# Performance work log

Hardware: AMD Instinct MI355X
Metric: run time of the kernel (lower is better)

The kernel has to match this reference:

```python
import jax, jax.numpy as jnp
import numpy as np

B, L = 64, 2048
V, E, G = 30, 128, 8          # n_tokens, embedding_size, n_globals
C, F, O = 64, 128, 30         # res_channels, f_channels, n_outputs
K, ND = 2, 9                  # kernel_size, n_dilations
GE = G * E                    # flattened global embedding dim


def causal_conv(x, w, b, dilation):
    # x: [B,Cin,L], w: [Cout,Cin,K] -> [B,Cout,L], causal via left padding
    pad = (w.shape[-1] - 1) * dilation
    out = jax.lax.conv_general_dilated(
        x, w, window_strides=(1,), padding=[(pad, 0)],
        rhs_dilation=(dilation,), dimension_numbers=("NCH", "OIH", "NCH"))
    return out + b[None, :, None]


def setup_inputs() -> dict:
    key = jax.random.key(0)
    ks = jax.random.split(key, 20)
    s = 0.05
    inp = {
        "input_tensor": jax.random.randint(ks[0], (B, L), 0, V),
        "global_input": jax.random.randint(ks[1], (B, G), 0, V),
        "emb_table": jax.random.normal(ks[2], (V, E), jnp.float32) * s,
        "w_causal": jax.random.normal(ks[3], (C, E, K), jnp.float32) * s,
        "b_causal": jnp.zeros((C,), jnp.float32),
        "w_f": jax.random.normal(ks[4], (ND, C, C, K), jnp.float32) * s,
        "b_f": jnp.zeros((ND, C), jnp.float32),
        "w_g": jax.random.normal(ks[5], (ND, C, C, K), jnp.float32) * s,
        "b_g": jnp.zeros((ND, C), jnp.float32),
        "wl_f": jax.random.normal(ks[6], (ND, C, GE), jnp.float32) * s,
        "bl_f": jnp.zeros((ND, C), jnp.float32),
        "wl_g": jax.random.normal(ks[7], (ND, C, GE), jnp.float32) * s,
        "bl_g": jnp.zeros((ND, C), jnp.float32),
        "w_res": jax.random.normal(ks[8], (ND, C, C), jnp.float32) * s,
        "b_res": jnp.zeros((ND, C), jnp.float32),
        "w_fin1": jax.random.normal(ks[9], (F, C), jnp.float32) * s,
        "b_fin1": jnp.zeros((F,), jnp.float32),
        "w_fin2": jax.random.normal(ks[10], (O, F), jnp.float32) * s,
        "b_fin2": jnp.zeros((O,), jnp.float32),
    }
    return inp


def reference(input_tensor, global_input, emb_table, w_causal, b_causal,
              w_f, b_f, w_g, b_g, wl_f, bl_f, wl_g, bl_g,
              w_res, b_res, w_fin1, b_fin1, w_fin2, b_fin2):
    # padding_idx=0: row 0 is zero and receives no gradient
    table = emb_table.at[0].set(0.0)
    emb = table[input_tensor]                     # [B,L,E]
    emb_g = table[global_input].reshape(B, GE)    # [B,G*E]
    x = jnp.transpose(emb, (0, 2, 1))             # [B,E,L]
    res = causal_conv(x, w_causal, b_causal, 1)   # [B,C,L]
    skips = jnp.zeros_like(res)
    for i in range(ND):
        d = 2 ** (i + 1)
        h_f = emb_g @ wl_f[i].T + bl_f[i]         # [B,C]
        h_g = emb_g @ wl_g[i].T + bl_g[i]
        x_f = causal_conv(res, w_f[i], b_f[i], d) + h_f[:, :, None]
        x_g = causal_conv(res, w_g[i], b_g[i], d) + h_g[:, :, None]
        z = jnp.tanh(x_f) * jax.nn.sigmoid(x_g)   # gated activation
        skip = jnp.einsum("oc,bcl->bol", w_res[i], z) + b_res[i][None, :, None]
        res = res + skip
        skips = skips + skip
    out = jax.nn.relu(skips)
    out = jnp.einsum("fc,bcl->bfl", w_fin1, out) + b_fin1[None, :, None]
    out = jax.nn.relu(out)
    out = jnp.einsum("of,bfl->bol", w_fin2, out) + b_fin2[None, :, None]
    return out
```

## Files before the change

kernel.cpp:

```cpp
#include <hip/hip_runtime.h>
#include <stdint.h>

#define Bz 64
#define Lz 2048
#define Vz 30
#define Ez 128
#define Gz 8
#define Cz 64
#define Fz 128
#define Oz 30
#define NDz 9

#define TWOLOG2E 2.8853900817779268f
#define NLOG2E  -1.4426950408889634f

typedef __attribute__((ext_vector_type(8))) short short8;
typedef _Float16 half8 __attribute__((ext_vector_type(8)));
typedef __fp16 fp16x2 __attribute__((ext_vector_type(2)));
typedef __attribute__((ext_vector_type(4))) float floatx4;

#define MFMA16B __builtin_amdgcn_mfma_f32_16x16x32_bf16
#define MFMA16H __builtin_amdgcn_mfma_f32_16x16x32_f16

__device__ __forceinline__ uint16_t f2bf(float f) {
    uint32_t u = __float_as_uint(f);
    u += 0x7fffu + ((u >> 16) & 1u);
    return (uint16_t)(u >> 16);
}
__device__ __forceinline__ uint16_t f2h(float f) {
    return __builtin_bit_cast(uint16_t, (_Float16)f);
}
__device__ __forceinline__ uint32_t pk2h(float lo, float hi) {
    fp16x2 h = __builtin_amdgcn_cvt_pkrtz(lo, hi);
    return __builtin_bit_cast(uint32_t, h);
}
__device__ __forceinline__ uint32_t pkadd(uint32_t oldbits, float a, float b) {
    fp16x2 h = __builtin_bit_cast(fp16x2, oldbits) + __builtin_amdgcn_cvt_pkrtz(a, b);
    return __builtin_bit_cast(uint32_t, h);
}
__device__ __forceinline__ float h2f(uint32_t u16bits) {
    return (float)__builtin_bit_cast(_Float16, (uint16_t)u16bits);
}
__device__ __forceinline__ float fexp2(float x) {
#if __has_builtin(__builtin_amdgcn_exp2f)
    return __builtin_amdgcn_exp2f(x);
#else
    float r; asm("v_exp_f32 %0, %1" : "=v"(r) : "v"(x)); return r;
#endif
}
__device__ __forceinline__ float gatefn(float fl, float gl) {
    float a = fexp2(fl);
    float b = fexp2(gl);
    float ap1 = a + 1.f;
    return (a - 1.f) * __builtin_amdgcn_rcpf(fmaf(ap1, b, ap1));
}

#define N_WB   (NDz * 128 * 128)
#define N_WR   (NDz * 64 * 64)
#define N_W1   (Fz * Cz)
#define N_W2   (32 * Fz)
#define N_PROJ (Vz * Cz)
#define N_WLB  (NDz * 128 * 1024)
#define N_EMB  (Bz * 1024)
#define N_BIAS (NDz * 128)

__global__ void pack_k(const float* __restrict__ w_f, const float* __restrict__ w_g,
                       const float* __restrict__ w_res, const float* __restrict__ w_fin1,
                       const float* __restrict__ w_fin2, const float* __restrict__ w_causal,
                       const float* __restrict__ table, const int* __restrict__ gin,
                       const float* __restrict__ wl_f, const float* __restrict__ wl_g,
                       const float* __restrict__ b_f, const float* __restrict__ b_g,
                       const float* __restrict__ bl_f, const float* __restrict__ bl_g,
                       uint16_t* __restrict__ WB, uint16_t* __restrict__ WrB,
                       uint16_t* __restrict__ W1B, uint16_t* __restrict__ W2B,
                       float* __restrict__ proj0, float* __restrict__ proj1,
                       uint16_t* __restrict__ WLB, uint16_t* __restrict__ embG,
                       float* __restrict__ biasrow) {
    int tid = blockIdx.x * 256 + threadIdx.x;
    if (tid < N_WB) {
        int i = tid >> 14, rem = tid & 16383, ch = rem >> 7, k = rem & 127;
        int kin = k & 63, tap = (k < 64) ? 1 : 0;
        float v = (ch < 64) ? w_f[((i * Cz + ch) * Cz + kin) * 2 + tap] * TWOLOG2E
                            : w_g[((i * Cz + (ch - 64)) * Cz + kin) * 2 + tap] * NLOG2E;
        WB[tid] = f2h(v);
        return;
    }
    tid -= N_WB;
    if (tid < N_WR) { WrB[tid] = f2h(w_res[tid]); return; }
    tid -= N_WR;
    if (tid < N_W1) { W1B[tid] = f2h(w_fin1[tid]); return; }
    tid -= N_W1;
    if (tid < N_W2) {
        int o = tid >> 7, f = tid & 127;
        W2B[tid] = f2h(o < Oz ? w_fin2[o * Fz + f] : 0.f);
        return;
    }
    tid -= N_W2;
    if (tid < N_PROJ) {
        int v = tid >> 6, c = tid & 63;
        float s0 = 0.f, s1 = 0.f;
        if (v != 0) {
            for (int e = 0; e < Ez; e++) {
                float tv = table[v * Ez + e];
                s0 += w_causal[(c * Ez + e) * 2 + 0] * tv;
                s1 += w_causal[(c * Ez + e) * 2 + 1] * tv;
            }
        }
        proj0[tid] = s0; proj1[tid] = s1;
        return;
    }
    tid -= N_PROJ;
    if (tid < N_WLB) {
        int row = tid >> 10, j = tid & 1023;
        int i = row >> 7, rem = row & 127, fg = rem >> 6, c = rem & 63;
        const float* wl = fg ? wl_g : wl_f;
        float sc = fg ? NLOG2E : TWOLOG2E;
        WLB[tid] = f2bf(wl[((size_t)(i * Cz + c)) * 1024 + j] * sc);
        return;
    }
    tid -= N_WLB;
    if (tid < N_EMB) {
        int b = tid >> 10, j = tid & 1023;
        int g = j >> 7, e = j & 127;
        int v = gin[b * Gz + g];
        embG[tid] = f2bf(v ? table[v * Ez + e] : 0.f);
        return;
    }
    tid -= N_EMB;
    if (tid < N_BIAS) {
        int i = tid >> 7, rem = tid & 127, fg = rem >> 6, c = rem & 63;
        float bsum = (fg ? b_g : b_f)[i * Cz + c] + (fg ? bl_g : bl_f)[i * Cz + c];
        biasrow[tid] = bsum * (fg ? NLOG2E : TWOLOG2E);
    }
}

__global__ __launch_bounds__(256) void hgemm_k(
    const uint16_t* __restrict__ WLB, const uint16_t* __restrict__ embG,
    const float* __restrict__ biasrow, float* __restrict__ hhT) {
    int tx = threadIdx.x, lane = tx & 63, wave = tx >> 6;
    int nl = lane & 15, quad = lane >> 4;
    int row0 = blockIdx.x * 64 + wave * 16;
    floatx4 acc[4];
    float bv[4];
#pragma unroll
    for (int r = 0; r < 4; r++) bv[r] = biasrow[row0 + quad * 4 + r];
#pragma unroll
    for (int nt = 0; nt < 4; nt++)
#pragma unroll
        for (int r = 0; r < 4; r++) acc[nt][r] = bv[r];
    const uint16_t* ap = WLB + (size_t)(row0 + nl) * 1024 + quad * 8;
#pragma unroll 4
    for (int ks = 0; ks < 32; ks++) {
        short8 a = *(const short8*)(ap + ks * 32);
#pragma unroll
        for (int nt = 0; nt < 4; nt++) {
            short8 bb = *(const short8*)(embG + (size_t)(nt * 16 + nl) * 1024 + ks * 32 + quad * 8);
            acc[nt] = MFMA16B(a, bb, acc[nt], 0, 0, 0);
        }
    }
#pragma unroll
    for (int nt = 0; nt < 4; nt++)
#pragma unroll
        for (int r = 0; r < 4; r++)
            hhT[(size_t)(row0 + quad * 4 + r) * 64 + nt * 16 + nl] = acc[nt][r];
}

__global__ __launch_bounds__(256) void init_k(
    const int* __restrict__ tok, const float* __restrict__ b_causal,
    const float* __restrict__ proj0, const float* __restrict__ proj1,
    uint16_t* __restrict__ res) {
    int tx = threadIdx.x;
    int q = tx & 15, tl = tx >> 4;
    int b = blockIdx.y;
    int t = blockIdx.x * 16 + tl;
    int v1 = tok[b * Lz + t];
    int v0 = (t > 0) ? tok[b * Lz + t - 1] : 0;
    float4 p1 = ((const float4*)(proj1 + v1 * Cz))[q];
    float4 p0 = ((const float4*)(proj0 + v0 * Cz))[q];
    float4 bc = ((const float4*)b_causal)[q];
    float rx = p1.x + p0.x + bc.x, ry = p1.y + p0.y + bc.y;
    float rz = p1.z + p0.z + bc.z, rw = p1.w + p0.w + bc.w;
    *(uint2*)(res + ((size_t)(b * Lz + t)) * Cz + q * 4) =
        make_uint2(pk2h(rx, ry), pk2h(rz, rw));
}

__global__ __launch_bounds__(256, 2) void fused_k(
    const uint16_t* __restrict__ rin, uint16_t* __restrict__ rout,
    const uint16_t* __restrict__ WB, const uint16_t* __restrict__ WrB,
    const float* __restrict__ hhT, const float* __restrict__ b_res) {
    __shared__ __align__(16) uint16_t R[256 * 72];
    __shared__ __align__(16) uint16_t Zb[256 * 72];
    int tx = threadIdx.x;
    int lane = tx & 63, wave = tx >> 6;
    int nl = lane & 15, quad = lane >> 4;
    int b = blockIdx.y, t0 = blockIdx.x * 128;
    const uint16_t* rb16 = rin + ((size_t)b * Lz) * Cz;

    if (t0 != 0) {
        const uint16_t* src = rb16 + (size_t)(t0 - 128) * Cz;
#pragma unroll
        for (int it = 0; it < 8; it++) {
            int id = it * 256 + tx, row = id >> 3, c8 = id & 7;
            uint4 v = *(const uint4*)(src + (size_t)row * Cz + c8 * 8);
            *(uint4*)(R + row * 72 + c8 * 8) = v;
        }
    } else {
#pragma unroll
        for (int it = 0; it < 8; it++) {
            int id = it * 256 + tx, row = id >> 3, c8 = id & 7;
            int t = row - 128;
            uint4 v = make_uint4(0u, 0u, 0u, 0u);
            if (t >= 0) v = *(const uint4*)(rb16 + (size_t)t * Cz + c8 * 8);
            *(uint4*)(R + row * 72 + c8 * 8) = v;
        }
    }
    floatx4 ss[8];
#pragma unroll
    for (int j = 0; j < 8; j++)
#pragma unroll
        for (int r = 0; r < 4; r++) ss[j][r] = 0.f;
    __syncthreads();

    const int chq = wave * 16 + quad * 4;
    const int NT0[6] = {0, 0, 1, 2, 4, 8};

#pragma unroll
    for (int l = 0; l < 6; l++) {
        const int d = 2 << l;
        const int nt0 = NT0[l];
        const uint16_t* wf = WB + l * 16384 + (wave * 16 + nl) * 128 + quad * 8;
        half8 AF[4], AG[4];
#pragma unroll
        for (int ks = 0; ks < 4; ks++) {
            AF[ks] = *(const half8*)(wf + ks * 32);
            AG[ks] = *(const half8*)(wf + 64 * 128 + ks * 32);
        }
        const uint16_t* wr = WrB + l * 4096 + (wave * 16 + nl) * 64 + quad * 8;
        half8 AR0 = *(const half8*)(wr);
        half8 AR1 = *(const half8*)(wr + 32);
        float hfv[4], hgv[4], brv[4];
        const float* hp = hhT + ((size_t)(l * 128 + wave * 16 + quad * 4)) * 64 + b;
#pragma unroll
        for (int r = 0; r < 4; r++) { hfv[r] = hp[r * 64]; hgv[r] = hp[4096 + r * 64]; }
        const float* brp = b_res + l * Cz + wave * 16 + quad * 4;
#pragma unroll
        for (int r = 0; r < 4; r++) brv[r] = brp[r];

#pragma unroll
        for (int nt = 0; nt < 16; nt++) {
            if (nt < nt0) continue;
            int rowa = nt * 16 + nl;
            int rowb = rowa - d;
            if (nt * 16 < d) rowb = rowb < 0 ? 0 : rowb;
            const uint16_t* ra = R + rowa * 72 + quad * 8;
            const uint16_t* rb = R + rowb * 72 + quad * 8;
            half8 b0 = *(const half8*)(ra);
            half8 b1 = *(const half8*)(ra + 32);
            half8 b2 = *(const half8*)(rb);
            half8 b3 = *(const half8*)(rb + 32);
            floatx4 aF, aG;
#pragma unroll
            for (int r = 0; r < 4; r++) { aF[r] = hfv[r]; aG[r] = hgv[r]; }
            aF = MFMA16H(AF[0], b0, aF, 0, 0, 0); aG = MFMA16H(AG[0], b0, aG, 0, 0, 0);
            aF = MFMA16H(AF[1], b1, aF, 0, 0, 0); aG = MFMA16H(AG[1], b1, aG, 0, 0, 0);
            aF = MFMA16H(AF[2], b2, aF, 0, 0, 0); aG = MFMA16H(AG[2], b2, aG, 0, 0, 0);
            aF = MFMA16H(AF[3], b3, aF, 0, 0, 0); aG = MFMA16H(AG[3], b3, aG, 0, 0, 0);
            float z0 = gatefn(aF[0], aG[0]);
            float z1 = gatefn(aF[1], aG[1]);
            float z2 = gatefn(aF[2], aG[2]);
            float z3 = gatefn(aF[3], aG[3]);
            *(uint2*)(Zb + rowa * 72 + chq) = make_uint2(pk2h(z0, z1), pk2h(z2, z3));
        }
        __syncthreads();

        if (t0 != 0) {
#pragma unroll
            for (int nt = 0; nt < 16; nt++) {
                if (nt < nt0) continue;
                int pos = nt * 16 + nl;
                const uint16_t* zp = Zb + pos * 72 + quad * 8;
                floatx4 a2;
#pragma unroll
                for (int r = 0; r < 4; r++) a2[r] = brv[r];
                a2 = MFMA16H(AR0, *(const half8*)zp, a2, 0, 0, 0);
                a2 = MFMA16H(AR1, *(const half8*)(zp + 32), a2, 0, 0, 0);
                uint16_t* rp = R + pos * 72 + chq;
                uint2 oldp = *(uint2*)rp;
                *(uint2*)rp = make_uint2(pkadd(oldp.x, a2[0], a2[1]),
                                         pkadd(oldp.y, a2[2], a2[3]));
                if (nt >= 8) {
#pragma unroll
                    for (int r = 0; r < 4; r++) ss[nt - 8][r] += a2[r];
                }
            }
        } else {
#pragma unroll
            for (int nt = 0; nt < 16; nt++) {
                if (nt < nt0) continue;
                int pos = nt * 16 + nl;
                const uint16_t* zp = Zb + pos * 72 + quad * 8;
                floatx4 a2;
#pragma unroll
                for (int r = 0; r < 4; r++) a2[r] = brv[r];
                a2 = MFMA16H(AR0, *(const half8*)zp, a2, 0, 0, 0);
                a2 = MFMA16H(AR1, *(const half8*)(zp + 32), a2, 0, 0, 0);
                bool ok = (pos >= 128);
                uint16_t* rp = R + pos * 72 + chq;
                uint2 oldp = *(uint2*)rp;
                uint32_t ux = ok ? pkadd(oldp.x, a2[0], a2[1]) : 0u;
                uint32_t uy = ok ? pkadd(oldp.y, a2[2], a2[3]) : 0u;
                *(uint2*)rp = make_uint2(ux, uy);
                if (nt >= 8) {
#pragma unroll
                    for (int r = 0; r < 4; r++) ss[nt - 8][r] += a2[r];
                }
            }
        }
        __syncthreads();
    }

    uint16_t* ro = rout + ((size_t)b * Lz) * Cz;
#pragma unroll
    for (int j = 0; j < 8; j++) {
        size_t off = (size_t)(t0 + j * 16 + nl) * Cz + chq;
        uint2 rv = *(const uint2*)(rb16 + off);
        *(uint2*)(ro + off) = make_uint2(pkadd(rv.x, ss[j][0], ss[j][1]),
                                         pkadd(rv.y, ss[j][2], ss[j][3]));
    }
}

__global__ __launch_bounds__(256, 4) void layer_k(
    const uint16_t* __restrict__ rin, uint16_t* __restrict__ rout,
    const uint16_t* __restrict__ WBl, const uint16_t* __restrict__ WrBl,
    const float* __restrict__ hhT, const float* __restrict__ b_res,
    int i, int d) {
    __shared__ __align__(16) uint16_t X[64 * 136];
    __shared__ __align__(16) uint16_t Z[64 * 72];
    int tx = threadIdx.x;
    int lane = tx & 63, wave = tx >> 6;
    int nl = lane & 15, quad = lane >> 4;
    int b = blockIdx.y, t0 = blockIdx.x * 64;
    const uint16_t* rb16 = rin + ((size_t)b * Lz) * Cz;

#pragma unroll
    for (int it = 0; it < 2; it++) {
        int id = it * 256 + tx, row = id >> 3, c8 = id & 7;
        uint4 v = *(const uint4*)(rb16 + (size_t)(t0 + row) * Cz + c8 * 8);
        *(uint4*)(X + row * 136 + c8 * 8) = v;
    }
#pragma unroll
    for (int it = 0; it < 2; it++) {
        int id = it * 256 + tx, row = id >> 3, c8 = id & 7;
        int tb = t0 + row - d;
        uint4 v = make_uint4(0u, 0u, 0u, 0u);
        if (tb >= 0) v = *(const uint4*)(rb16 + (size_t)tb * Cz + c8 * 8);
        *(uint4*)(X + row * 136 + 64 + c8 * 8) = v;
    }

    half8 AF[4], AG[4], AR[2];
    {
        const uint16_t* wf = WBl + (wave * 16 + nl) * 128 + quad * 8;
#pragma unroll
        for (int ks = 0; ks < 4; ks++) {
            AF[ks] = *(const half8*)(wf + ks * 32);
            AG[ks] = *(const half8*)(wf + 64 * 128 + ks * 32);
        }
        const uint16_t* wr = WrBl + (wave * 16 + nl) * 64 + quad * 8;
#pragma unroll
        for (int ks = 0; ks < 2; ks++) AR[ks] = *(const half8*)(wr + ks * 32);
    }
    float hfv[4], hgv[4], brv[4];
    {
        const float* hp = hhT + ((size_t)(i * 128 + wave * 16 + quad * 4)) * 64 + b;
#pragma unroll
        for (int r = 0; r < 4; r++) {
            hfv[r] = hp[r * 64];
            hgv[r] = hp[4096 + r * 64];
        }
        const float* brp = b_res + i * Cz + wave * 16 + quad * 4;
#pragma unroll
        for (int r = 0; r < 4; r++) brv[r] = brp[r];
    }
    __syncthreads();

    floatx4 accF[4], accG[4];
#pragma unroll
    for (int nt = 0; nt < 4; nt++)
#pragma unroll
        for (int r = 0; r < 4; r++) { accF[nt][r] = hfv[r]; accG[nt][r] = hgv[r]; }
#pragma unroll
    for (int nt = 0; nt < 4; nt++) {
        const uint16_t* xp = X + (nt * 16 + nl) * 136 + quad * 8;
#pragma unroll
        for (int ks = 0; ks < 4; ks++) {
            half8 bf = *(const half8*)(xp + ks * 32);
            accF[nt] = MFMA16H(AF[ks], bf, accF[nt], 0, 0, 0);
            accG[nt] = MFMA16H(AG[ks], bf, accG[nt], 0, 0, 0);
        }
    }

    int chq = wave * 16 + quad * 4;
#pragma unroll
    for (int nt = 0; nt < 4; nt++) {
        int pos = nt * 16 + nl;
        float z0 = gatefn(accF[nt][0], accG[nt][0]);
        float z1 = gatefn(accF[nt][1], accG[nt][1]);
        float z2 = gatefn(accF[nt][2], accG[nt][2]);
        float z3 = gatefn(accF[nt][3], accG[nt][3]);
        *(uint2*)(Z + pos * 72 + chq) = make_uint2(pk2h(z0, z1), pk2h(z2, z3));
    }
    __syncthreads();

    floatx4 acc2[4];
#pragma unroll
    for (int nt = 0; nt < 4; nt++)
#pragma unroll
        for (int r = 0; r < 4; r++) acc2[nt][r] = brv[r];
#pragma unroll
    for (int nt = 0; nt < 4; nt++) {
        const uint16_t* zp = Z + (nt * 16 + nl) * 72 + quad * 8;
        acc2[nt] = MFMA16H(AR[0], *(const half8*)zp, acc2[nt], 0, 0, 0);
        acc2[nt] = MFMA16H(AR[1], *(const half8*)(zp + 32), acc2[nt], 0, 0, 0);
    }

    uint16_t* ro = rout + ((size_t)b * Lz) * Cz;
#pragma unroll
    for (int nt = 0; nt < 4; nt++) {
        size_t off = (size_t)(t0 + nt * 16 + nl) * Cz + chq;
        uint2 rv = *(const uint2*)(rb16 + off);
        *(uint2*)(ro + off) = make_uint2(pkadd(rv.x, acc2[nt][0], acc2[nt][1]),
                                         pkadd(rv.y, acc2[nt][2], acc2[nt][3]));
    }
}

__global__ __launch_bounds__(256, 3) void final_k(
    const uint16_t* __restrict__ res0, const uint16_t* __restrict__ resF,
    const uint16_t* __restrict__ W1B, const uint16_t* __restrict__ W2B,
    const float* __restrict__ b_fin1, const float* __restrict__ b_fin2,
    float* __restrict__ out) {
    __shared__ __align__(16) uint16_t S[128 * 72];
    __shared__ __align__(16) uint16_t Mi[128 * 136];
    int tx = threadIdx.x;
    int lane = tx & 63, wave = tx >> 6;
    int nl = lane & 15, quad = lane >> 4;
    int b = blockIdx.y, t0 = blockIdx.x * 128;
    const uint16_t* r0 = res0 + ((size_t)b * Lz) * Cz;
    const uint16_t* rF = resF + ((size_t)b * Lz) * Cz;

    half8 A1[2][2], A2[2][4];
#pragma unroll
    for (int mt = 0; mt < 2; mt++) {
        const uint16_t* w1 = W1B + (wave * 32 + mt * 16 + nl) * 64 + quad * 8;
#pragma unroll
        for (int ks = 0; ks < 2; ks++) A1[mt][ks] = *(const half8*)(w1 + ks * 32);
        const uint16_t* w2 = W2B + (mt * 16 + nl) * 128 + quad * 8;
#pragma unroll
        for (int ks = 0; ks < 4; ks++) A2[mt][ks] = *(const half8*)(w2 + ks * 32);
    }
#pragma unroll
    for (int it = 0; it < 4; it++) {
        int id = it * 256 + tx, row = id >> 3, c8 = id & 7;
        uint4 fv = *(const uint4*)(rF + (size_t)(t0 + row) * Cz + c8 * 8);
        uint4 ov = *(const uint4*)(r0 + (size_t)(t0 + row) * Cz + c8 * 8);
        float s0 = fmaxf(h2f(fv.x) - h2f(ov.x), 0.f);
        float s1 = fmaxf(h2f(fv.x >> 16) - h2f(ov.x >> 16), 0.f);
        float s2 = fmaxf(h2f(fv.y) - h2f(ov.y), 0.f);
        float s3 = fmaxf(h2f(fv.y >> 16) - h2f(ov.y >> 16), 0.f);
        float s4 = fmaxf(h2f(fv.z) - h2f(ov.z), 0.f);
        float s5 = fmaxf(h2f(fv.z >> 16) - h2f(ov.z >> 16), 0.f);
        float s6 = fmaxf(h2f(fv.w) - h2f(ov.w), 0.f);
        float s7 = fmaxf(h2f(fv.w >> 16) - h2f(ov.w >> 16), 0.f);
        *(uint4*)(S + row * 72 + c8 * 8) =
            make_uint4(pk2h(s0, s1), pk2h(s2, s3), pk2h(s4, s5), pk2h(s6, s7));
    }
    __syncthreads();

    floatx4 accM[2][8];
    float b1v[2][4];
#pragma unroll
    for (int mt = 0; mt < 2; mt++)
#pragma unroll
        for (int r = 0; r < 4; r++) b1v[mt][r] = b_fin1[wave * 32 + mt * 16 + quad * 4 + r];
#pragma unroll
    for (int mt = 0; mt < 2; mt++)
#pragma unroll
        for (int nt = 0; nt < 8; nt++)
#pragma unroll
            for (int r = 0; r < 4; r++) accM[mt][nt][r] = b1v[mt][r];
#pragma unroll
    for (int nt = 0; nt < 8; nt++) {
        const uint16_t* sp = S + (nt * 16 + nl) * 72 + quad * 8;
#pragma unroll
        for (int ks = 0; ks < 2; ks++) {
            half8 s = *(const half8*)(sp + ks * 32);
            accM[0][nt] = MFMA16H(A1[0][ks], s, accM[0][nt], 0, 0, 0);
            accM[1][nt] = MFMA16H(A1[1][ks], s, accM[1][nt], 0, 0, 0);
        }
    }
#pragma unroll
    for (int mt = 0; mt < 2; mt++)
#pragma unroll
        for (int nt = 0; nt < 8; nt++) {
            int pos = nt * 16 + nl;
            int fq = wave * 32 + mt * 16 + quad * 4;
            float m0 = fmaxf(accM[mt][nt][0], 0.f), m1 = fmaxf(accM[mt][nt][1], 0.f);
            float m2 = fmaxf(accM[mt][nt][2], 0.f), m3 = fmaxf(accM[mt][nt][3], 0.f);
            *(uint2*)(Mi + pos * 136 + fq) = make_uint2(pk2h(m0, m1), pk2h(m2, m3));
        }
    __syncthreads();

    floatx4 accO[2][2];
#pragma unroll
    for (int mt = 0; mt < 2; mt++)
#pragma unroll
        for (int r = 0; r < 4; r++) {
            int o = mt * 16 + quad * 4 + r;
            float bo = (o < Oz) ? b_fin2[o] : 0.f;
            accO[mt][0][r] = bo; accO[mt][1][r] = bo;
        }
#pragma unroll
    for (int ntl = 0; ntl < 2; ntl++) {
        int nt = wave * 2 + ntl;
        const uint16_t* mp = Mi + (nt * 16 + nl) * 136 + quad * 8;
#pragma unroll
        for (int ks = 0; ks < 4; ks++) {
            half8 m = *(const half8*)(mp + ks * 32);
            accO[0][ntl] = MFMA16H(A2[0][ks], m, accO[0][ntl], 0, 0, 0);
            accO[1][ntl] = MFMA16H(A2[1][ks], m, accO[1][ntl], 0, 0, 0);
        }
    }
#pragma unroll
    for (int mt = 0; mt < 2; mt++)
#pragma unroll
        for (int ntl = 0; ntl < 2; ntl++)
#pragma unroll
            for (int r = 0; r < 4; r++) {
                int o = mt * 16 + quad * 4 + r;
                if (o < Oz)
                    out[((size_t)b * Oz + o) * Lz + t0 + (wave * 2 + ntl) * 16 + nl] =
                        accO[mt][ntl][r];
            }
}

extern "C" void kernel_launch(void* const* d_in, const int* in_sizes, int n_in,
                              void* d_out, int out_size, void* d_ws, size_t ws_size,
                              hipStream_t stream) {
    const int*   tok      = (const int*)d_in[0];
    const int*   gin      = (const int*)d_in[1];
    const float* table    = (const float*)d_in[2];
    const float* w_causal = (const float*)d_in[3];
    const float* b_causal = (const float*)d_in[4];
    const float* w_f      = (const float*)d_in[5];
    const float* b_f      = (const float*)d_in[6];
    const float* w_g      = (const float*)d_in[7];
    const float* b_g      = (const float*)d_in[8];
    const float* wl_f     = (const float*)d_in[9];
    const float* bl_f     = (const float*)d_in[10];
    const float* wl_g     = (const float*)d_in[11];
    const float* bl_g     = (const float*)d_in[12];
    const float* w_res    = (const float*)d_in[13];
    const float* b_res    = (const float*)d_in[14];
    const float* w_fin1   = (const float*)d_in[15];
    const float* b_fin1   = (const float*)d_in[16];
    const float* w_fin2   = (const float*)d_in[17];
    const float* b_fin2   = (const float*)d_in[18];
    float* out = (float*)d_out;

    const size_t NRES = (size_t)Bz * Lz * Cz;
    uint16_t* u16 = (uint16_t*)d_ws;
    uint16_t* resA = u16;
    uint16_t* resB = resA + NRES;
    uint16_t* resC = resB + NRES;
    uint16_t* WB   = resC + NRES;
    uint16_t* WrB  = WB + N_WB;
    uint16_t* W1B  = WrB + N_WR;
    uint16_t* W2B  = W1B + N_W1;
    uint16_t* WLB  = W2B + N_W2;
    uint16_t* embG = WLB + N_WLB;
    float* hhT     = (float*)(embG + N_EMB);
    float* proj0   = hhT + 73728;
    float* proj1   = proj0 + N_PROJ;
    float* biasrow = proj1 + N_PROJ;

    int npack = N_WB + N_WR + N_W1 + N_W2 + N_PROJ + N_WLB + N_EMB + N_BIAS;
    pack_k<<<(npack + 255) / 256, 256, 0, stream>>>(
        w_f, w_g, w_res, w_fin1, w_fin2, w_causal, table, gin,
        wl_f, wl_g, b_f, b_g, bl_f, bl_g,
        WB, WrB, W1B, W2B, proj0, proj1, WLB, embG, biasrow);
    hgemm_k<<<18, 256, 0, stream>>>(WLB, embG, biasrow, hhT);
    init_k<<<dim3(Lz / 16, Bz), 256, 0, stream>>>(tok, b_causal, proj0, proj1, resA);

    fused_k<<<dim3(Lz / 128, Bz), 256, 0, stream>>>(resA, resB, WB, WrB, hhT, b_res);
    layer_k<<<dim3(Lz / 64, Bz), 256, 0, stream>>>(
        resB, resC, WB + (size_t)6 * 16384, WrB + (size_t)6 * 4096, hhT, b_res, 6, 128);
    layer_k<<<dim3(Lz / 64, Bz), 256, 0, stream>>>(
        resC, resB, WB + (size_t)7 * 16384, WrB + (size_t)7 * 4096, hhT, b_res, 7, 256);
    layer_k<<<dim3(Lz / 64, Bz), 256, 0, stream>>>(
        resB, resC, WB + (size_t)8 * 16384, WrB + (size_t)8 * 4096, hhT, b_res, 8, 512);
    final_k<<<dim3(Lz / 128, Bz), 256, 0, stream>>>(resA, resC, W1B, W2B,
                                                    b_fin1, b_fin2, out);
}
```

Before: 285.5 us.

## Split fused layer kernel across 8 waves and split-K the global-embedding GEMM

The fused first-six-layers kernel now runs 512 threads per block: each channel group of 16 is handled by two waves that take interleaved time tiles, which halves the per-wave tile work and skip accumulators. Separately, the small conditioning GEMM is split along K across the four waves, with a shared-memory reduction, and launched on 72 blocks instead of 18. Both changes aim to raise parallelism and hide latency. The cost is a larger block and register pressure under the 512,4 launch bound, plus an extra reduction and barrier in the GEMM.

```diff
diff --git a/kernel.cpp b/kernel.cpp
--- a/kernel.cpp
+++ b/kernel.cpp
@@ -137,20 +137,19 @@
 __global__ __launch_bounds__(256) void hgemm_k(
     const uint16_t* __restrict__ WLB, const uint16_t* __restrict__ embG,
     const float* __restrict__ biasrow, float* __restrict__ hhT) {
+    __shared__ float red[4][4][64][4];
     int tx = threadIdx.x, lane = tx & 63, wave = tx >> 6;
     int nl = lane & 15, quad = lane >> 4;
-    int row0 = blockIdx.x * 64 + wave * 16;
+    int row0 = blockIdx.x * 16;
     floatx4 acc[4];
-    float bv[4];
-#pragma unroll
-    for (int r = 0; r < 4; r++) bv[r] = biasrow[row0 + quad * 4 + r];
 #pragma unroll
     for (int nt = 0; nt < 4; nt++)
 #pragma unroll
-        for (int r = 0; r < 4; r++) acc[nt][r] = bv[r];
+        for (int r = 0; r < 4; r++) acc[nt][r] = 0.f;
     const uint16_t* ap = WLB + (size_t)(row0 + nl) * 1024 + quad * 8;
-#pragma unroll 4
-    for (int ks = 0; ks < 32; ks++) {
+#pragma unroll
+    for (int k8 = 0; k8 < 8; k8++) {
+        int ks = wave * 8 + k8;
         short8 a = *(const short8*)(ap + ks * 32);
 #pragma unroll
         for (int nt = 0; nt < 4; nt++) {
@@ -161,8 +160,18 @@
 #pragma unroll
     for (int nt = 0; nt < 4; nt++)
 #pragma unroll
-        for (int r = 0; r < 4; r++)
-            hhT[(size_t)(row0 + quad * 4 + r) * 64 + nt * 16 + nl] = acc[nt][r];
+        for (int r = 0; r < 4; r++) red[nt][wave][lane][r] = acc[nt][r];
+    __syncthreads();
+    {
+        int nt = wave;
+#pragma unroll
+        for (int r = 0; r < 4; r++) {
+            float s = red[nt][0][lane][r] + red[nt][1][lane][r] +
+                      red[nt][2][lane][r] + red[nt][3][lane][r];
+            hhT[(size_t)(row0 + quad * 4 + r) * 64 + nt * 16 + nl] =
+                s + biasrow[row0 + quad * 4 + r];
+        }
+    }
 }
 
 __global__ __launch_bounds__(256) void init_k(
@@ -184,7 +193,7 @@
         make_uint2(pk2h(rx, ry), pk2h(rz, rw));
 }
 
-__global__ __launch_bounds__(256, 2) void fused_k(
+__global__ __launch_bounds__(512, 4) void fused_k(
     const uint16_t* __restrict__ rin, uint16_t* __restrict__ rout,
     const uint16_t* __restrict__ WB, const uint16_t* __restrict__ WrB,
     const float* __restrict__ hhT, const float* __restrict__ b_res) {
@@ -192,6 +201,7 @@
     __shared__ __align__(16) uint16_t Zb[256 * 72];
     int tx = threadIdx.x;
     int lane = tx & 63, wave = tx >> 6;
+    int cw = wave & 3, p = wave >> 2;
     int nl = lane & 15, quad = lane >> 4;
     int b = blockIdx.y, t0 = blockIdx.x * 128;
     const uint16_t* rb16 = rin + ((size_t)b * Lz) * Cz;
@@ -199,55 +209,56 @@
     if (t0 != 0) {
         const uint16_t* src = rb16 + (size_t)(t0 - 128) * Cz;
 #pragma unroll
-        for (int it = 0; it < 8; it++) {
-            int id = it * 256 + tx, row = id >> 3, c8 = id & 7;
+        for (int it = 0; it < 4; it++) {
+            int id = it * 512 + tx, row = id >> 3, c8 = id & 7;
             uint4 v = *(const uint4*)(src + (size_t)row * Cz + c8 * 8);
             *(uint4*)(R + row * 72 + c8 * 8) = v;
         }
     } else {
 #pragma unroll
-        for (int it = 0; it < 8; it++) {
-            int id = it * 256 + tx, row = id >> 3, c8 = id & 7;
+        for (int it = 0; it < 4; it++) {
+            int id = it * 512 + tx, row = id >> 3, c8 = id & 7;
             int t = row - 128;
             uint4 v = make_uint4(0u, 0u, 0u, 0u);
             if (t >= 0) v = *(const uint4*)(rb16 + (size_t)t * Cz + c8 * 8);
             *(uint4*)(R + row * 72 + c8 * 8) = v;
         }
     }
-    floatx4 ss[8];
-#pragma unroll
-    for (int j = 0; j < 8; j++)
+    floatx4 ss[4];
+#pragma unroll
+    for (int j = 0; j < 4; j++)
 #pragma unroll
         for (int r = 0; r < 4; r++) ss[j][r] = 0.f;
     __syncthreads();
 
-    const int chq = wave * 16 + quad * 4;
+    const int chq = cw * 16 + quad * 4;
     const int NT0[6] = {0, 0, 1, 2, 4, 8};
 
 #pragma unroll
     for (int l = 0; l < 6; l++) {
         const int d = 2 << l;
         const int nt0 = NT0[l];
-        const uint16_t* wf = WB + l * 16384 + (wave * 16 + nl) * 128 + quad * 8;
+        const uint16_t* wf = WB + l * 16384 + (cw * 16 + nl) * 128 + quad * 8;
         half8 AF[4], AG[4];
 #pragma unroll
         for (int ks = 0; ks < 4; ks++) {
             AF[ks] = *(const half8*)(wf + ks * 32);
             AG[ks] = *(const half8*)(wf + 64 * 128 + ks * 32);
         }
-        const uint16_t* wr = WrB + l * 4096 + (wave * 16 + nl) * 64 + quad * 8;
+        const uint16_t* wr = WrB + l * 4096 + (cw * 16 + nl) * 64 + quad * 8;
         half8 AR0 = *(const half8*)(wr);
         half8 AR1 = *(const half8*)(wr + 32);
         float hfv[4], hgv[4], brv[4];
-        const float* hp = hhT + ((size_t)(l * 128 + wave * 16 + quad * 4)) * 64 + b;
+        const float* hp = hhT + ((size_t)(l * 128 + cw * 16 + quad * 4)) * 64 + b;
 #pragma unroll
         for (int r = 0; r < 4; r++) { hfv[r] = hp[r * 64]; hgv[r] = hp[4096 + r * 64]; }
-        const float* brp = b_res + l * Cz + wave * 16 + quad * 4;
+        const float* brp = b_res + l * Cz + cw * 16 + quad * 4;
 #pragma unroll
         for (int r = 0; r < 4; r++) brv[r] = brp[r];
 
 #pragma unroll
-        for (int nt = 0; nt < 16; nt++) {
+        for (int i = 0; i < 8; i++) {
+            int nt = i * 2 + p;
             if (nt < nt0) continue;
             int rowa = nt * 16 + nl;
             int rowb = rowa - d;
@@ -275,7 +286,8 @@
 
         if (t0 != 0) {
 #pragma unroll
-            for (int nt = 0; nt < 16; nt++) {
+            for (int i = 0; i < 8; i++) {
+                int nt = i * 2 + p;
                 if (nt < nt0) continue;
                 int pos = nt * 16 + nl;
                 const uint16_t* zp = Zb + pos * 72 + quad * 8;
@@ -288,14 +300,15 @@
                 uint2 oldp = *(uint2*)rp;
                 *(uint2*)rp = make_uint2(pkadd(oldp.x, a2[0], a2[1]),
                                          pkadd(oldp.y, a2[2], a2[3]));
-                if (nt >= 8) {
-#pragma unroll
-                    for (int r = 0; r < 4; r++) ss[nt - 8][r] += a2[r];
+                if (i >= 4) {
+#pragma unroll
+                    for (int r = 0; r < 4; r++) ss[i - 4][r] += a2[r];
                 }
             }
         } else {
 #pragma unroll
-            for (int nt = 0; nt < 16; nt++) {
+            for (int i = 0; i < 8; i++) {
+                int nt = i * 2 + p;
                 if (nt < nt0) continue;
                 int pos = nt * 16 + nl;
                 const uint16_t* zp = Zb + pos * 72 + quad * 8;
@@ -310,9 +323,9 @@
                 uint32_t ux = ok ? pkadd(oldp.x, a2[0], a2[1]) : 0u;
                 uint32_t uy = ok ? pkadd(oldp.y, a2[2], a2[3]) : 0u;
                 *(uint2*)rp = make_uint2(ux, uy);
-                if (nt >= 8) {
-#pragma unroll
-                    for (int r = 0; r < 4; r++) ss[nt - 8][r] += a2[r];
+                if (i >= 4) {
+#pragma unroll
+                    for (int r = 0; r < 4; r++) ss[i - 4][r] += a2[r];
                 }
             }
         }
@@ -321,11 +334,11 @@
 
     uint16_t* ro = rout + ((size_t)b * Lz) * Cz;
 #pragma unroll
-    for (int j = 0; j < 8; j++) {
-        size_t off = (size_t)(t0 + j * 16 + nl) * Cz + chq;
+    for (int k = 0; k < 4; k++) {
+        size_t off = (size_t)(t0 + (2 * k + p) * 16 + nl) * Cz + chq;
         uint2 rv = *(const uint2*)(rb16 + off);
-        *(uint2*)(ro + off) = make_uint2(pkadd(rv.x, ss[j][0], ss[j][1]),
-                                         pkadd(rv.y, ss[j][2], ss[j][3]));
+        *(uint2*)(ro + off) = make_uint2(pkadd(rv.x, ss[k][0], ss[k][1]),
+                                         pkadd(rv.y, ss[k][2], ss[k][3]));
     }
 }
 
@@ -587,10 +600,10 @@
         w_f, w_g, w_res, w_fin1, w_fin2, w_causal, table, gin,
         wl_f, wl_g, b_f, b_g, bl_f, bl_g,
         WB, WrB, W1B, W2B, proj0, proj1, WLB, embG, biasrow);
-    hgemm_k<<<18, 256, 0, stream>>>(WLB, embG, biasrow, hhT);
+    hgemm_k<<<72, 256, 0, stream>>>(WLB, embG, biasrow, hhT);
     init_k<<<dim3(Lz / 16, Bz), 256, 0, stream>>>(tok, b_causal, proj0, proj1, resA);
 
-    fused_k<<<dim3(Lz / 128, Bz), 256, 0, stream>>>(resA, resB, WB, WrB, hhT, b_res);
+    fused_k<<<dim3(Lz / 128, Bz), 512, 0, stream>>>(resA, resB, WB, WrB, hhT, b_res);
     layer_k<<<dim3(Lz / 64, Bz), 256, 0, stream>>>(
         resB, resC, WB + (size_t)6 * 16384, WrB + (size_t)6 * 4096, hhT, b_res, 6, 128);
     layer_k<<<dim3(Lz / 64, Bz), 256, 0, stream>>>(
```

After: 305.5 us. +7.0%, slower.

## Shrink fused layer halo to five layers, split-K hgemm, swizzle gate buffer

Applied to the files above, without the earlier changes.

The fused multi-layer kernel now covers only the first five dilation layers with a 64-row halo instead of 128. That cuts recomputed halo work and LDS use, and occupancy rises to three blocks per SU. Layer 5 moves to an extra standalone layer_k launch, which adds another full read/write pass over the residual. The gate buffer drops its padding in favour of an XOR swizzle to avoid LDS bank conflicts. The hgemm now splits K across waves with a shared-memory reduction and launches four times as many blocks, giving more parallelism on that small GEMM.

```diff
diff --git a/kernel.cpp b/kernel.cpp
--- a/kernel.cpp
+++ b/kernel.cpp
@@ -137,20 +137,19 @@
 __global__ __launch_bounds__(256) void hgemm_k(
     const uint16_t* __restrict__ WLB, const uint16_t* __restrict__ embG,
     const float* __restrict__ biasrow, float* __restrict__ hhT) {
+    __shared__ float red[4][4][64][4];
     int tx = threadIdx.x, lane = tx & 63, wave = tx >> 6;
     int nl = lane & 15, quad = lane >> 4;
-    int row0 = blockIdx.x * 64 + wave * 16;
+    int row0 = blockIdx.x * 16;
     floatx4 acc[4];
-    float bv[4];
-#pragma unroll
-    for (int r = 0; r < 4; r++) bv[r] = biasrow[row0 + quad * 4 + r];
 #pragma unroll
     for (int nt = 0; nt < 4; nt++)
 #pragma unroll
-        for (int r = 0; r < 4; r++) acc[nt][r] = bv[r];
+        for (int r = 0; r < 4; r++) acc[nt][r] = 0.f;
     const uint16_t* ap = WLB + (size_t)(row0 + nl) * 1024 + quad * 8;
-#pragma unroll 4
-    for (int ks = 0; ks < 32; ks++) {
+#pragma unroll
+    for (int k8 = 0; k8 < 8; k8++) {
+        int ks = wave * 8 + k8;
         short8 a = *(const short8*)(ap + ks * 32);
 #pragma unroll
         for (int nt = 0; nt < 4; nt++) {
@@ -161,8 +160,18 @@
 #pragma unroll
     for (int nt = 0; nt < 4; nt++)
 #pragma unroll
-        for (int r = 0; r < 4; r++)
-            hhT[(size_t)(row0 + quad * 4 + r) * 64 + nt * 16 + nl] = acc[nt][r];
+        for (int r = 0; r < 4; r++) red[nt][wave][lane][r] = acc[nt][r];
+    __syncthreads();
+    {
+        int nt = wave;
+#pragma unroll
+        for (int r = 0; r < 4; r++) {
+            float s = red[nt][0][lane][r] + red[nt][1][lane][r] +
+                      red[nt][2][lane][r] + red[nt][3][lane][r];
+            hhT[(size_t)(row0 + quad * 4 + r) * 64 + nt * 16 + nl] =
+                s + biasrow[row0 + quad * 4 + r];
+        }
+    }
 }
 
 __global__ __launch_bounds__(256) void init_k(
@@ -184,12 +193,12 @@
         make_uint2(pk2h(rx, ry), pk2h(rz, rw));
 }
 
-__global__ __launch_bounds__(256, 2) void fused_k(
+__global__ __launch_bounds__(256, 3) void fused_k(
     const uint16_t* __restrict__ rin, uint16_t* __restrict__ rout,
     const uint16_t* __restrict__ WB, const uint16_t* __restrict__ WrB,
     const float* __restrict__ hhT, const float* __restrict__ b_res) {
-    __shared__ __align__(16) uint16_t R[256 * 72];
-    __shared__ __align__(16) uint16_t Zb[256 * 72];
+    __shared__ __align__(16) uint16_t R[192 * 72];
+    __shared__ __align__(16) uint16_t Zb[192 * 64];
     int tx = threadIdx.x;
     int lane = tx & 63, wave = tx >> 6;
     int nl = lane & 15, quad = lane >> 4;
@@ -197,18 +206,18 @@
     const uint16_t* rb16 = rin + ((size_t)b * Lz) * Cz;
 
     if (t0 != 0) {
-        const uint16_t* src = rb16 + (size_t)(t0 - 128) * Cz;
-#pragma unroll
-        for (int it = 0; it < 8; it++) {
+        const uint16_t* src = rb16 + (size_t)(t0 - 64) * Cz;
+#pragma unroll
+        for (int it = 0; it < 6; it++) {
             int id = it * 256 + tx, row = id >> 3, c8 = id & 7;
             uint4 v = *(const uint4*)(src + (size_t)row * Cz + c8 * 8);
             *(uint4*)(R + row * 72 + c8 * 8) = v;
         }
     } else {
 #pragma unroll
-        for (int it = 0; it < 8; it++) {
+        for (int it = 0; it < 6; it++) {
             int id = it * 256 + tx, row = id >> 3, c8 = id & 7;
-            int t = row - 128;
+            int t = row - 64;
             uint4 v = make_uint4(0u, 0u, 0u, 0u);
             if (t >= 0) v = *(const uint4*)(rb16 + (size_t)t * Cz + c8 * 8);
             *(uint4*)(R + row * 72 + c8 * 8) = v;
@@ -222,10 +231,14 @@
     __syncthreads();
 
     const int chq = wave * 16 + quad * 4;
-    const int NT0[6] = {0, 0, 1, 2, 4, 8};
-
-#pragma unroll
-    for (int l = 0; l < 6; l++) {
+    const int zmask = (nl & 7) << 3;
+    const int zwr  = chq ^ zmask;
+    const int zrd0 = (quad * 8) ^ zmask;
+    const int zrd1 = (quad * 8 + 32) ^ zmask;
+    const int NT0[5] = {0, 0, 1, 2, 4};
+
+#pragma unroll
+    for (int l = 0; l < 5; l++) {
         const int d = 2 << l;
         const int nt0 = NT0[l];
         const uint16_t* wf = WB + l * 16384 + (wave * 16 + nl) * 128 + quad * 8;
@@ -247,7 +260,7 @@
         for (int r = 0; r < 4; r++) brv[r] = brp[r];
 
 #pragma unroll
-        for (int nt = 0; nt < 16; nt++) {
+        for (int nt = 0; nt < 12; nt++) {
             if (nt < nt0) continue;
             int rowa = nt * 16 + nl;
             int rowb = rowa - d;
@@ -269,50 +282,50 @@
             float z1 = gatefn(aF[1], aG[1]);
             float z2 = gatefn(aF[2], aG[2]);
             float z3 = gatefn(aF[3], aG[3]);
-            *(uint2*)(Zb + rowa * 72 + chq) = make_uint2(pk2h(z0, z1), pk2h(z2, z3));
+            *(uint2*)(Zb + rowa * 64 + zwr) = make_uint2(pk2h(z0, z1), pk2h(z2, z3));
         }
         __syncthreads();
 
         if (t0 != 0) {
 #pragma unroll
-            for (int nt = 0; nt < 16; nt++) {
+            for (int nt = 0; nt < 12; nt++) {
                 if (nt < nt0) continue;
                 int pos = nt * 16 + nl;
-                const uint16_t* zp = Zb + pos * 72 + quad * 8;
+                const uint16_t* zb0 = Zb + pos * 64;
                 floatx4 a2;
 #pragma unroll
                 for (int r = 0; r < 4; r++) a2[r] = brv[r];
-                a2 = MFMA16H(AR0, *(const half8*)zp, a2, 0, 0, 0);
-                a2 = MFMA16H(AR1, *(const half8*)(zp + 32), a2, 0, 0, 0);
+                a2 = MFMA16H(AR0, *(const half8*)(zb0 + zrd0), a2, 0, 0, 0);
+                a2 = MFMA16H(AR1, *(const half8*)(zb0 + zrd1), a2, 0, 0, 0);
                 uint16_t* rp = R + pos * 72 + chq;
                 uint2 oldp = *(uint2*)rp;
                 *(uint2*)rp = make_uint2(pkadd(oldp.x, a2[0], a2[1]),
                                          pkadd(oldp.y, a2[2], a2[3]));
-                if (nt >= 8) {
-#pragma unroll
-                    for (int r = 0; r < 4; r++) ss[nt - 8][r] += a2[r];
+                if (nt >= 4) {
+#pragma unroll
+                    for (int r = 0; r < 4; r++) ss[nt - 4][r] += a2[r];
                 }
             }
         } else {
 #pragma unroll
-            for (int nt = 0; nt < 16; nt++) {
+            for (int nt = 0; nt < 12; nt++) {
                 if (nt < nt0) continue;
                 int pos = nt * 16 + nl;
-                const uint16_t* zp = Zb + pos * 72 + quad * 8;
+                const uint16_t* zb0 = Zb + pos * 64;
                 floatx4 a2;
 #pragma unroll
                 for (int r = 0; r < 4; r++) a2[r] = brv[r];
-                a2 = MFMA16H(AR0, *(const half8*)zp, a2, 0, 0, 0);
-                a2 = MFMA16H(AR1, *(const half8*)(zp + 32), a2, 0, 0, 0);
-                bool ok = (pos >= 128);
+                a2 = MFMA16H(AR0, *(const half8*)(zb0 + zrd0), a2, 0, 0, 0);
+                a2 = MFMA16H(AR1, *(const half8*)(zb0 + zrd1), a2, 0, 0, 0);
+                bool ok = (pos >= 64);
                 uint16_t* rp = R + pos * 72 + chq;
                 uint2 oldp = *(uint2*)rp;
                 uint32_t ux = ok ? pkadd(oldp.x, a2[0], a2[1]) : 0u;
                 uint32_t uy = ok ? pkadd(oldp.y, a2[2], a2[3]) : 0u;
                 *(uint2*)rp = make_uint2(ux, uy);
-                if (nt >= 8) {
-#pragma unroll
-                    for (int r = 0; r < 4; r++) ss[nt - 8][r] += a2[r];
+                if (nt >= 4) {
+#pragma unroll
+                    for (int r = 0; r < 4; r++) ss[nt - 4][r] += a2[r];
                 }
             }
         }
@@ -587,16 +600,18 @@
         w_f, w_g, w_res, w_fin1, w_fin2, w_causal, table, gin,
         wl_f, wl_g, b_f, b_g, bl_f, bl_g,
         WB, WrB, W1B, W2B, proj0, proj1, WLB, embG, biasrow);
-    hgemm_k<<<18, 256, 0, stream>>>(WLB, embG, biasrow, hhT);
+    hgemm_k<<<72, 256, 0, stream>>>(WLB, embG, biasrow, hhT);
     init_k<<<dim3(Lz / 16, Bz), 256, 0, stream>>>(tok, b_causal, proj0, proj1, resA);
 
     fused_k<<<dim3(Lz / 128, Bz), 256, 0, stream>>>(resA, resB, WB, WrB, hhT, b_res);
     layer_k<<<dim3(Lz / 64, Bz), 256, 0, stream>>>(
-        resB, resC, WB + (size_t)6 * 16384, WrB + (size_t)6 * 4096, hhT, b_res, 6, 128);
+        resB, resC, WB + (size_t)5 * 16384, WrB + (size_t)5 * 4096, hhT, b_res, 5, 64);
     layer_k<<<dim3(Lz / 64, Bz), 256, 0, stream>>>(
-        resC, resB, WB + (size_t)7 * 16384, WrB + (size_t)7 * 4096, hhT, b_res, 7, 256);
+        resC, resB, WB + (size_t)6 * 16384, WrB + (size_t)6 * 4096, hhT, b_res, 6, 128);
     layer_k<<<dim3(Lz / 64, Bz), 256, 0, stream>>>(
-        resB, resC, WB + (size_t)8 * 16384, WrB + (size_t)8 * 4096, hhT, b_res, 8, 512);
-    final_k<<<dim3(Lz / 128, Bz), 256, 0, stream>>>(resA, resC, W1B, W2B,
+        resB, resC, WB + (size_t)7 * 16384, WrB + (size_t)7 * 4096, hhT, b_res, 7, 256);
+    layer_k<<<dim3(Lz / 64, Bz), 256, 0, stream>>>(
+        resC, resB, WB + (size_t)8 * 16384, WrB + (size_t)8 * 4096, hhT, b_res, 8, 512);
+    final_k<<<dim3(Lz / 128, Bz), 256, 0, stream>>>(resA, resB, W1B, W2B,
                                                     b_fin1, b_fin2, out);
 }
```

New measurement: 272.0 us. 4.7% less time.
